# Kernel optimization log

Hardware: AMD Instinct MI355X
Metric: run time of the kernel (lower is better)

Reference implementation:

```python
import jax, jax.numpy as jnp
import numpy as np

N, X_DIM, Y_DIM, HID = 1024, 128, 128, 256


def setup_inputs() -> dict:
    key = jax.random.key(0)
    k1, k2, k3, k4 = jax.random.split(key, 4)
    return {
        "x_samples": jax.random.normal(k1, (N, X_DIM), dtype=jnp.float32),
        "y_samples": jax.random.normal(k2, (N, Y_DIM), dtype=jnp.float32),
        "W1": jax.random.normal(k3, (X_DIM + Y_DIM, HID), dtype=jnp.float32) * 0.05,
        "b1": jnp.zeros((HID,), dtype=jnp.float32),
        "W2": jax.random.normal(k4, (HID, 1), dtype=jnp.float32) * 0.05,
        "b2": jnp.zeros((1,), dtype=jnp.float32),
    }


def reference(x_samples, y_samples, W1, b1, W2, b2):
    n = y_samples.shape[0]
    x_dim = x_samples.shape[-1]
    # Split first linear so we never materialize the N^2 concat:
    W1x, W1y = W1[:x_dim], W1[x_dim:]
    pre_x = x_samples @ W1x  # [N, H]
    pre_y = y_samples @ W1y  # [N, H]
    # T0: F on matched pairs (x_i, y_i)
    T0 = jax.nn.relu(pre_x + pre_y + b1) @ W2 + b2  # [N, 1]
    # T1[i, j] = F([x_j, y_i]) - 1.0  (all-pairs grid)
    h = jax.nn.relu(pre_x[None, :, :] + pre_y[:, None, :] + b1)  # [N, N, H]
    T1 = h @ W2 + b2 - 1.0  # [N, N, 1]
    lse = jax.nn.logsumexp(T1, axis=1)  # [N, 1]
    lower_bound = T0.mean() - jnp.exp(lse - jnp.log(jnp.float32(n))).mean()
    return lower_bound
```

## Files before the change

kernel.cpp:

```cpp
#include <hip/hip_runtime.h>

typedef _Float16 h2 __attribute__((ext_vector_type(2)));
typedef unsigned int u32;

#define OFF_XP   0u
#define OFF_YP   0x40000u
#define OFF_W1XP 0x80000u
#define OFF_W1YP 0x90000u
#define OFF_A2   0x100000u
#define OFF_C2   0x180000u

__device__ __forceinline__ u32 pack2(float a, float b) {
  h2 v; v.x = (_Float16)a; v.y = (_Float16)b;
  return __builtin_bit_cast(u32, v);
}
__device__ __forceinline__ h2 as_h2(u32 u) { return __builtin_bit_cast(h2, u); }

__device__ __forceinline__ float fdot2(h2 a, h2 b, float c) {
#if __has_builtin(__builtin_amdgcn_fdot2)
  return __builtin_amdgcn_fdot2(a, b, c, false);
#else
  return (float)a.x * (float)b.x + (float)a.y * (float)b.y + c;
#endif
}
__device__ __forceinline__ h2 relu2(h2 t) {
  h2 z; z.x = (_Float16)0.0f; z.y = (_Float16)0.0f;
  return __builtin_elementwise_max(t, z);
}

__global__ void k0_pack(const float* __restrict__ x, const float* __restrict__ y,
                        const float* __restrict__ W1, u32* __restrict__ wsu,
                        float* __restrict__ out) {
  const int b = blockIdx.x, tid = threadIdx.x;
  if (b == 0 && tid == 0) out[0] = 0.0f;
  if (b < 128) {
    const float* src = (b < 64) ? x : y;
    u32* dst = wsu + ((b < 64) ? (OFF_XP >> 2) : (OFF_YP >> 2));
    const int bb = b & 63, kt = bb & 3, rt = bb >> 2;
    __shared__ float sT[64][33];
    const int kl = tid & 31, rg = tid >> 5;
#pragma unroll
    for (int p = 0; p < 8; ++p) {
      const int r = p * 8 + rg;
      sT[r][kl] = src[(rt * 64 + r) * 128 + kt * 32 + kl];
    }
    __syncthreads();
    const int rl = tid & 63, kg = tid >> 6;
#pragma unroll
    for (int q = 0; q < 4; ++q) {
      const int kkl = q * 4 + kg;
      dst[(kt * 16 + kkl) * 1024 + rt * 64 + rl] =
          pack2(sT[rl][2 * kkl], sT[rl][2 * kkl + 1]);
    }
  } else {
    const int kk = b - 128, h = tid;
    wsu[(OFF_W1XP >> 2) + kk * 256 + h] =
        pack2(W1[(2 * kk) * 256 + h], W1[(2 * kk + 1) * 256 + h]);
    wsu[(OFF_W1YP >> 2) + kk * 256 + h] =
        pack2(W1[(128 + 2 * kk) * 256 + h], W1[(129 + 2 * kk) * 256 + h]);
  }
}

__global__ __launch_bounds__(256) void k1_pre(u32* __restrict__ wsu,
                                              const float* __restrict__ b1) {
  const int b = blockIdx.x, tid = threadIdx.x;
  const int mat = b >> 8;
  const int bb = b & 255, ht = bb & 7, rt = bb >> 3;
  const int tx = tid & 31, ty = tid >> 5;
  const int h0 = ht * 32 + ty * 4;
  const u32* xp  = wsu + (mat ? (OFF_YP >> 2) : (OFF_XP >> 2)) + rt * 32 + tx;
  const u32* w1p = wsu + (mat ? (OFF_W1YP >> 2) : (OFF_W1XP >> 2)) + h0;
  u32* dst = wsu + (mat ? (OFF_C2 >> 2) : (OFF_A2 >> 2)) + rt * 4096 + tx * 128;

  float acc[4];
  if (mat) {
    const float4 bv = *(const float4*)(b1 + h0);
    acc[0] = bv.x; acc[1] = bv.y; acc[2] = bv.z; acc[3] = bv.w;
  } else {
    acc[0] = acc[1] = acc[2] = acc[3] = 0.0f;
  }

  u32 XR[8]; uint4 WR[8];
#pragma unroll
  for (int s = 0; s < 8; ++s) {
    XR[s] = xp[s * 1024];
    WR[s] = *(const uint4*)(w1p + s * 256);
  }
#pragma unroll 8
  for (int kk = 0; kk < 56; ++kk) {
    const int s = kk & 7;
    const h2 xr = as_h2(XR[s]); const uint4 wv = WR[s];
    XR[s] = xp[(kk + 8) * 1024];
    WR[s] = *(const uint4*)(w1p + (kk + 8) * 256);
    acc[0] = fdot2(xr, as_h2(wv.x), acc[0]);
    acc[1] = fdot2(xr, as_h2(wv.y), acc[1]);
    acc[2] = fdot2(xr, as_h2(wv.z), acc[2]);
    acc[3] = fdot2(xr, as_h2(wv.w), acc[3]);
  }
#pragma unroll
  for (int kk = 56; kk < 64; ++kk) {
    const int s = kk & 7;
    const h2 xr = as_h2(XR[s]); const uint4 wv = WR[s];
    acc[0] = fdot2(xr, as_h2(wv.x), acc[0]);
    acc[1] = fdot2(xr, as_h2(wv.y), acc[1]);
    acc[2] = fdot2(xr, as_h2(wv.z), acc[2]);
    acc[3] = fdot2(xr, as_h2(wv.w), acc[3]);
  }
  const int hh0 = ht * 16 + ty * 2;
  uint2 sv;
  sv.x = pack2(acc[0], acc[1]);
  sv.y = pack2(acc[2], acc[3]);
  *(uint2*)(dst + hh0) = sv;
}

__global__ __launch_bounds__(256) void k2_main(const u32* __restrict__ wsu,
                                               const float* __restrict__ W2g,
                                               const float* __restrict__ B2,
                                               float* __restrict__ out) {
  const int bi = blockIdx.x >> 5, bj = blockIdx.x & 31;
  const int tid = threadIdx.x;
  const int tx = tid & 15, ty = tid >> 4;

  __shared__ uint4 sA4[32 * 32];
  __shared__ uint4 sC4[32 * 32];
  __shared__ uint4 sW4[32];
  __shared__ float sred[4];
  u32* sW2 = (u32*)sW4;

  {
    const u32* gA = wsu + (OFF_A2 >> 2) + bj * 4096;
    const u32* gC = wsu + (OFF_C2 >> 2) + bi * 4096;
    const int j = tid >> 3, q8 = tid & 7, sw = (j >> 1) & 7;
#pragma unroll
    for (int m = 0; m < 4; ++m) {
      const int q = q8 + 8 * m;
      sA4[j * 32 + (q ^ sw)] = *(const uint4*)(gA + j * 128 + q * 4);
      sC4[j * 32 + (q ^ sw)] = *(const uint4*)(gC + j * 128 + q * 4);
    }
    if (tid < 128) sW2[tid] = pack2(W2g[2 * tid], W2g[2 * tid + 1]);
  }
  __syncthreads();

  const uint4* rA0 = sA4 + (2 * tx) * 32;
  const uint4* rA1 = rA0 + 32;
  const uint4* rC0 = sC4 + (2 * ty) * 32;
  const uint4* rC1 = rC0 + 32;
  const int swzA = tx & 7, swzC = ty & 7;

  float acc[4] = {0.0f, 0.0f, 0.0f, 0.0f};
#pragma unroll 4
  for (int g = 0; g < 32; ++g) {
    const uint4 av0 = rA0[g ^ swzA], av1 = rA1[g ^ swzA];
    const uint4 cv0 = rC0[g ^ swzC], cv1 = rC1[g ^ swzC];
    const uint4 wv = sW4[g];
    const u32 a0[4] = {av0.x, av0.y, av0.z, av0.w};
    const u32 a1[4] = {av1.x, av1.y, av1.z, av1.w};
    const u32 c0[4] = {cv0.x, cv0.y, cv0.z, cv0.w};
    const u32 c1[4] = {cv1.x, cv1.y, cv1.z, cv1.w};
    const u32 ww[4] = {wv.x, wv.y, wv.z, wv.w};
#pragma unroll
    for (int m = 0; m < 4; ++m) {
      const h2 A0 = as_h2(a0[m]), A1 = as_h2(a1[m]);
      const h2 C0 = as_h2(c0[m]), C1 = as_h2(c1[m]);
      const h2 w = as_h2(ww[m]);
      acc[0] = fdot2(relu2(A0 + C0), w, acc[0]);
      acc[1] = fdot2(relu2(A1 + C0), w, acc[1]);
      acc[2] = fdot2(relu2(A0 + C1), w, acc[2]);
      acc[3] = fdot2(relu2(A1 + C1), w, acc[3]);
    }
  }

  const float b2 = B2[0];
  float val = 0.0f;
#pragma unroll
  for (int p = 0; p < 4; ++p) val += __expf(acc[p] + (b2 - 1.0f));
  val *= -1.0f / 1048576.0f;
  if (bi == bj && tx == ty)
    val += (acc[0] + acc[3] + 2.0f * b2) * (1.0f / 1024.0f);
#pragma unroll
  for (int off = 32; off > 0; off >>= 1) val += __shfl_down(val, off, 64);
  if ((tid & 63) == 0) sred[tid >> 6] = val;
  __syncthreads();
  if (tid == 0) atomicAdd(out, sred[0] + sred[1] + sred[2] + sred[3]);
}

extern "C" void kernel_launch(void* const* d_in, const int* in_sizes, int n_in,
                              void* d_out, int out_size, void* d_ws, size_t ws_size,
                              hipStream_t stream) {
  const float* x  = (const float*)d_in[0];
  const float* y  = (const float*)d_in[1];
  const float* W1 = (const float*)d_in[2];
  const float* b1 = (const float*)d_in[3];
  const float* W2 = (const float*)d_in[4];
  const float* b2 = (const float*)d_in[5];
  u32* wsu = (u32*)d_ws;

  hipLaunchKernelGGL(k0_pack, dim3(192), dim3(256), 0, stream, x, y, W1, wsu,
                     (float*)d_out);
  hipLaunchKernelGGL(k1_pre, dim3(512), dim3(256), 0, stream, wsu, b1);
  hipLaunchKernelGGL(k2_main, dim3(1024), dim3(256), 0, stream, wsu, W2, b2,
                     (float*)d_out);
}
```

Baseline: 89.55 us.

## Fuse pack into pre-GEMM via LDS staging and enlarge main-kernel tile to 64x32

Drops the separate packing kernel. The pre-activation kernel now loads fp32 x/y and W1 tiles directly into swizzled LDS and accumulates in fp32, which saves one launch and a workspace round trip. The main kernel now computes a 4x2 output block per thread (64x32 per block), halving the grid and reusing each A vector across more C rows to reduce LDS traffic per FMA. The costs are higher register use and LDS footprint, fewer blocks to fill the CUs, and a different diagonal-detection logic for T0.

Measured after the change: 86.98 us. 1.03x faster.

```diff
diff --git a/kernel.cpp b/kernel.cpp
--- a/kernel.cpp
+++ b/kernel.cpp
@@ -3,10 +3,6 @@
 typedef _Float16 h2 __attribute__((ext_vector_type(2)));
 typedef unsigned int u32;
 
-#define OFF_XP   0u
-#define OFF_YP   0x40000u
-#define OFF_W1XP 0x80000u
-#define OFF_W1YP 0x90000u
 #define OFF_A2   0x100000u
 #define OFF_C2   0x180000u
 
@@ -28,84 +24,61 @@
   return __builtin_elementwise_max(t, z);
 }
 
-__global__ void k0_pack(const float* __restrict__ x, const float* __restrict__ y,
-                        const float* __restrict__ W1, u32* __restrict__ wsu,
-                        float* __restrict__ out) {
+__global__ __launch_bounds__(256) void k1_pre(const float* __restrict__ x,
+                                              const float* __restrict__ y,
+                                              const float* __restrict__ W1,
+                                              const float* __restrict__ b1,
+                                              u32* __restrict__ wsu,
+                                              float* __restrict__ out) {
   const int b = blockIdx.x, tid = threadIdx.x;
   if (b == 0 && tid == 0) out[0] = 0.0f;
-  if (b < 128) {
-    const float* src = (b < 64) ? x : y;
-    u32* dst = wsu + ((b < 64) ? (OFF_XP >> 2) : (OFF_YP >> 2));
-    const int bb = b & 63, kt = bb & 3, rt = bb >> 2;
-    __shared__ float sT[64][33];
-    const int kl = tid & 31, rg = tid >> 5;
-#pragma unroll
-    for (int p = 0; p < 8; ++p) {
-      const int r = p * 8 + rg;
-      sT[r][kl] = src[(rt * 64 + r) * 128 + kt * 32 + kl];
-    }
-    __syncthreads();
-    const int rl = tid & 63, kg = tid >> 6;
-#pragma unroll
-    for (int q = 0; q < 4; ++q) {
-      const int kkl = q * 4 + kg;
-      dst[(kt * 16 + kkl) * 1024 + rt * 64 + rl] =
-          pack2(sT[rl][2 * kkl], sT[rl][2 * kkl + 1]);
-    }
-  } else {
-    const int kk = b - 128, h = tid;
-    wsu[(OFF_W1XP >> 2) + kk * 256 + h] =
-        pack2(W1[(2 * kk) * 256 + h], W1[(2 * kk + 1) * 256 + h]);
-    wsu[(OFF_W1YP >> 2) + kk * 256 + h] =
-        pack2(W1[(128 + 2 * kk) * 256 + h], W1[(129 + 2 * kk) * 256 + h]);
-  }
-}
-
-__global__ __launch_bounds__(256) void k1_pre(u32* __restrict__ wsu,
-                                              const float* __restrict__ b1) {
-  const int b = blockIdx.x, tid = threadIdx.x;
   const int mat = b >> 8;
   const int bb = b & 255, ht = bb & 7, rt = bb >> 3;
+
+  __shared__ float4 sx4[32 * 32];
+  __shared__ float  sw[128 * 32];
+
+  const float* gx = (mat ? y : x) + rt * 32 * 128;
+  const float* gw = W1 + mat * (128 * 256) + ht * 32;
+
+#pragma unroll
+  for (int p = 0; p < 4; ++p) {
+    const int idx = p * 256 + tid, r = idx >> 5, q = idx & 31;
+    sx4[r * 32 + (q ^ (r & 7))] = *(const float4*)(gx + r * 128 + q * 4);
+  }
+#pragma unroll
+  for (int p = 0; p < 4; ++p) {
+    const int kr = p * 32 + (tid >> 3), c4 = (tid & 7) * 4;
+    *(float4*)(sw + kr * 32 + c4) = *(const float4*)(gw + kr * 256 + c4);
+  }
+  __syncthreads();
+
   const int tx = tid & 31, ty = tid >> 5;
-  const int h0 = ht * 32 + ty * 4;
-  const u32* xp  = wsu + (mat ? (OFF_YP >> 2) : (OFF_XP >> 2)) + rt * 32 + tx;
-  const u32* w1p = wsu + (mat ? (OFF_W1YP >> 2) : (OFF_W1XP >> 2)) + h0;
-  u32* dst = wsu + (mat ? (OFF_C2 >> 2) : (OFF_A2 >> 2)) + rt * 4096 + tx * 128;
+  const int h0 = ty * 4;
 
   float acc[4];
   if (mat) {
-    const float4 bv = *(const float4*)(b1 + h0);
+    const float4 bv = *(const float4*)(b1 + ht * 32 + h0);
     acc[0] = bv.x; acc[1] = bv.y; acc[2] = bv.z; acc[3] = bv.w;
   } else {
     acc[0] = acc[1] = acc[2] = acc[3] = 0.0f;
   }
 
-  u32 XR[8]; uint4 WR[8];
+  const float4* xr = sx4 + tx * 32;
+  const int swx = tx & 7;
+#pragma unroll 8
+  for (int k4 = 0; k4 < 32; ++k4) {
+    const float4 xv = xr[k4 ^ swx];
+    const float xs[4] = {xv.x, xv.y, xv.z, xv.w};
 #pragma unroll
-  for (int s = 0; s < 8; ++s) {
-    XR[s] = xp[s * 1024];
-    WR[s] = *(const uint4*)(w1p + s * 256);
+    for (int kk = 0; kk < 4; ++kk) {
+      const float4 wv = *(const float4*)(sw + (4 * k4 + kk) * 32 + h0);
+      acc[0] += xs[kk] * wv.x; acc[1] += xs[kk] * wv.y;
+      acc[2] += xs[kk] * wv.z; acc[3] += xs[kk] * wv.w;
+    }
   }
-#pragma unroll 8
-  for (int kk = 0; kk < 56; ++kk) {
-    const int s = kk & 7;
-    const h2 xr = as_h2(XR[s]); const uint4 wv = WR[s];
-    XR[s] = xp[(kk + 8) * 1024];
-    WR[s] = *(const uint4*)(w1p + (kk + 8) * 256);
-    acc[0] = fdot2(xr, as_h2(wv.x), acc[0]);
-    acc[1] = fdot2(xr, as_h2(wv.y), acc[1]);
-    acc[2] = fdot2(xr, as_h2(wv.z), acc[2]);
-    acc[3] = fdot2(xr, as_h2(wv.w), acc[3]);
-  }
-#pragma unroll
-  for (int kk = 56; kk < 64; ++kk) {
-    const int s = kk & 7;
-    const h2 xr = as_h2(XR[s]); const uint4 wv = WR[s];
-    acc[0] = fdot2(xr, as_h2(wv.x), acc[0]);
-    acc[1] = fdot2(xr, as_h2(wv.y), acc[1]);
-    acc[2] = fdot2(xr, as_h2(wv.z), acc[2]);
-    acc[3] = fdot2(xr, as_h2(wv.w), acc[3]);
-  }
+
+  u32* dst = wsu + ((mat ? OFF_C2 : OFF_A2) >> 2) + rt * 4096 + tx * 128;
   const int hh0 = ht * 16 + ty * 2;
   uint2 sv;
   sv.x = pack2(acc[0], acc[1]);
@@ -119,64 +92,77 @@
                                                float* __restrict__ out) {
   const int bi = blockIdx.x >> 5, bj = blockIdx.x & 31;
   const int tid = threadIdx.x;
-  const int tx = tid & 15, ty = tid >> 4;
+  const int tx = tid & 15, TY = tid >> 4;
 
   __shared__ uint4 sA4[32 * 32];
-  __shared__ uint4 sC4[32 * 32];
+  __shared__ uint4 sC4[64 * 32];
   __shared__ uint4 sW4[32];
   __shared__ float sred[4];
   u32* sW2 = (u32*)sW4;
 
   {
     const u32* gA = wsu + (OFF_A2 >> 2) + bj * 4096;
-    const u32* gC = wsu + (OFF_C2 >> 2) + bi * 4096;
-    const int j = tid >> 3, q8 = tid & 7, sw = (j >> 1) & 7;
+    const u32* gC = wsu + (OFF_C2 >> 2) + bi * 8192;
 #pragma unroll
-    for (int m = 0; m < 4; ++m) {
-      const int q = q8 + 8 * m;
-      sA4[j * 32 + (q ^ sw)] = *(const uint4*)(gA + j * 128 + q * 4);
-      sC4[j * 32 + (q ^ sw)] = *(const uint4*)(gC + j * 128 + q * 4);
+    for (int p = 0; p < 4; ++p) {
+      const int idx = p * 256 + tid, j = idx >> 5, q = idx & 31;
+      sA4[j * 32 + (q ^ ((j >> 1) & 7))] = *(const uint4*)(gA + j * 128 + q * 4);
+    }
+#pragma unroll
+    for (int p = 0; p < 8; ++p) {
+      const int idx = p * 256 + tid, i = idx >> 5, q = idx & 31;
+      sC4[i * 32 + (q ^ ((i >> 2) & 7))] = *(const uint4*)(gC + i * 128 + q * 4);
     }
     if (tid < 128) sW2[tid] = pack2(W2g[2 * tid], W2g[2 * tid + 1]);
   }
   __syncthreads();
 
-  const uint4* rA0 = sA4 + (2 * tx) * 32;
-  const uint4* rA1 = rA0 + 32;
-  const uint4* rC0 = sC4 + (2 * ty) * 32;
-  const uint4* rC1 = rC0 + 32;
-  const int swzA = tx & 7, swzC = ty & 7;
+  const uint4* rA = sA4 + (2 * tx) * 32;
+  const uint4* rC = sC4 + (4 * TY) * 32;
+  const int swzA = tx & 7, swzC = TY & 7;
 
-  float acc[4] = {0.0f, 0.0f, 0.0f, 0.0f};
+  float acc[4][2] = {{0.0f, 0.0f}, {0.0f, 0.0f}, {0.0f, 0.0f}, {0.0f, 0.0f}};
 #pragma unroll 4
   for (int g = 0; g < 32; ++g) {
-    const uint4 av0 = rA0[g ^ swzA], av1 = rA1[g ^ swzA];
-    const uint4 cv0 = rC0[g ^ swzC], cv1 = rC1[g ^ swzC];
-    const uint4 wv = sW4[g];
-    const u32 a0[4] = {av0.x, av0.y, av0.z, av0.w};
-    const u32 a1[4] = {av1.x, av1.y, av1.z, av1.w};
-    const u32 c0[4] = {cv0.x, cv0.y, cv0.z, cv0.w};
-    const u32 c1[4] = {cv1.x, cv1.y, cv1.z, cv1.w};
+    const int ga = g ^ swzA, gc = g ^ swzC;
+    const uint4 av0 = rA[ga],      av1 = rA[32 + ga];
+    const uint4 cv0 = rC[gc],      cv1 = rC[32 + gc];
+    const uint4 cv2 = rC[64 + gc], cv3 = rC[96 + gc];
+    const uint4 wv  = sW4[g];
+    const u32 aa[2][4] = {{av0.x, av0.y, av0.z, av0.w},
+                          {av1.x, av1.y, av1.z, av1.w}};
+    const u32 cc[4][4] = {{cv0.x, cv0.y, cv0.z, cv0.w},
+                          {cv1.x, cv1.y, cv1.z, cv1.w},
+                          {cv2.x, cv2.y, cv2.z, cv2.w},
+                          {cv3.x, cv3.y, cv3.z, cv3.w}};
     const u32 ww[4] = {wv.x, wv.y, wv.z, wv.w};
 #pragma unroll
-    for (int m = 0; m < 4; ++m) {
-      const h2 A0 = as_h2(a0[m]), A1 = as_h2(a1[m]);
-      const h2 C0 = as_h2(c0[m]), C1 = as_h2(c1[m]);
-      const h2 w = as_h2(ww[m]);
-      acc[0] = fdot2(relu2(A0 + C0), w, acc[0]);
-      acc[1] = fdot2(relu2(A1 + C0), w, acc[1]);
-      acc[2] = fdot2(relu2(A0 + C1), w, acc[2]);
-      acc[3] = fdot2(relu2(A1 + C1), w, acc[3]);
+    for (int q = 0; q < 4; ++q) {
+      const h2 w = as_h2(ww[q]);
+      const h2 A0 = as_h2(aa[0][q]), A1 = as_h2(aa[1][q]);
+#pragma unroll
+      for (int m = 0; m < 4; ++m) {
+        const h2 C = as_h2(cc[m][q]);
+        acc[m][0] = fdot2(relu2(A0 + C), w, acc[m][0]);
+        acc[m][1] = fdot2(relu2(A1 + C), w, acc[m][1]);
+      }
     }
   }
 
   const float b2 = B2[0];
   float val = 0.0f;
 #pragma unroll
-  for (int p = 0; p < 4; ++p) val += __expf(acc[p] + (b2 - 1.0f));
+  for (int m = 0; m < 4; ++m)
+#pragma unroll
+    for (int p = 0; p < 2; ++p) val += __expf(acc[m][p] + (b2 - 1.0f));
   val *= -1.0f / 1048576.0f;
-  if (bi == bj && tx == ty)
-    val += (acc[0] + acc[3] + 2.0f * b2) * (1.0f / 1024.0f);
+  const int i0 = bi * 64 + 4 * TY, j0 = bj * 32 + 2 * tx;
+#pragma unroll
+  for (int m = 0; m < 4; ++m)
+#pragma unroll
+    for (int p = 0; p < 2; ++p)
+      if (i0 + m == j0 + p) val += (acc[m][p] + b2) * (1.0f / 1024.0f);
+
 #pragma unroll
   for (int off = 32; off > 0; off >>= 1) val += __shfl_down(val, off, 64);
   if ((tid & 63) == 0) sred[tid >> 6] = val;
@@ -195,9 +181,8 @@
   const float* b2 = (const float*)d_in[5];
   u32* wsu = (u32*)d_ws;
 
-  hipLaunchKernelGGL(k0_pack, dim3(192), dim3(256), 0, stream, x, y, W1, wsu,
+  hipLaunchKernelGGL(k1_pre, dim3(512), dim3(256), 0, stream, x, y, W1, b1, wsu,
                      (float*)d_out);
-  hipLaunchKernelGGL(k1_pre, dim3(512), dim3(256), 0, stream, wsu, b1);
-  hipLaunchKernelGGL(k2_main, dim3(1024), dim3(256), 0, stream, wsu, W2, b2,
+  hipLaunchKernelGGL(k2_main, dim3(512), dim3(256), 0, stream, wsu, W2, b2,
                      (float*)d_out);
 }
```
